# Optimization experiments

Hardware: AMD Instinct MI355X
Metric: run time of the kernel (lower is better)

The kernel has to match this reference:

```python
import jax, jax.numpy as jnp
import numpy as np

B, T, H = 1024, 1024, 64


def _lstm_cell(x, h, c, w_ih, w_hh, b_ih, b_hh):
    # gates: [B, 4H] in PyTorch order i, f, g, o
    g = x @ w_ih.T + h @ w_hh.T + b_ih + b_hh
    i, f, gg, o = jnp.split(g, 4, axis=-1)
    i = jax.nn.sigmoid(i)
    f = jax.nn.sigmoid(f)
    gg = jnp.tanh(gg)
    o = jax.nn.sigmoid(o)
    c_new = f * c + i * gg
    h_new = o * jnp.tanh(c_new)
    return h_new, c_new


def setup_inputs() -> dict:
    key = jax.random.key(0)
    ks = jax.random.split(key, 12)
    s = 1.0 / np.sqrt(H)  # torch default init scale
    r = lambda k, shape: jax.random.normal(k, shape, dtype=jnp.float32) * s
    return {
        "x": jax.random.normal(ks[0], (B, T), dtype=jnp.float32),
        "w_ih1": r(ks[1], (4 * H, 1)),
        "w_hh1": r(ks[2], (4 * H, H)),
        "b_ih1": r(ks[3], (4 * H,)),
        "b_hh1": r(ks[4], (4 * H,)),
        "w_ih2": r(ks[5], (4 * H, H)),
        "w_hh2": r(ks[6], (4 * H, H)),
        "b_ih2": r(ks[7], (4 * H,)),
        "b_hh2": r(ks[8], (4 * H,)),
        "w_lin": r(ks[9], (1, H)),
        "b_lin": r(ks[10], (1,)),
        "future_preds": 0,
    }


def reference(x, w_ih1, w_hh1, b_ih1, b_hh1, w_ih2, w_hh2, b_ih2, b_hh2,
              w_lin, b_lin, future_preds):
    bsz = x.shape[0]
    h1 = jnp.zeros((bsz, H), x.dtype)
    c1 = jnp.zeros((bsz, H), x.dtype)
    h2 = jnp.zeros((bsz, H), x.dtype)
    c2 = jnp.zeros((bsz, H), x.dtype)

    def step(carry, x_t):
        h1, c1, h2, c2 = carry
        h1, c1 = _lstm_cell(x_t, h1, c1, w_ih1, w_hh1, b_ih1, b_hh1)
        h2, c2 = _lstm_cell(h1, h2, c2, w_ih2, w_hh2, b_ih2, b_hh2)
        out = h2 @ w_lin.T + b_lin  # [B, 1]
        return (h1, c1, h2, c2), out

    xs = x.T[:, :, None]  # [T, B, 1]
    carry, outs = jax.lax.scan(step, (h1, c1, h2, c2), xs)
    outputs = outs[:, :, 0].T  # [B, T]

    if future_preds > 0:
        last = outs[-1]  # [B, 1]

        def fstep(carry, _):
            h1, c1, h2, c2, prev = carry
            h1, c1 = _lstm_cell(prev, h1, c1, w_ih1, w_hh1, b_ih1, b_hh1)
            h2, c2 = _lstm_cell(h1, h2, c2, w_ih2, w_hh2, b_ih2, b_hh2)
            out = h2 @ w_lin.T + b_lin
            return (h1, c1, h2, c2, out), out

        _, fouts = jax.lax.scan(fstep, (*carry, last), None, length=future_preds)
        outputs = jnp.concatenate([outputs, fouts[:, :, 0].T], axis=1)

    return outputs
```

## Files before the change

### kernel.cpp

```cpp
#include <hip/hip_runtime.h>
#include <hip/hip_bf16.h>


typedef _Float16 f16x8 __attribute__((ext_vector_type(8)));
typedef float    f32x4 __attribute__((ext_vector_type(4)));

namespace {
constexpr int Bb = 1024;
constexpr int Tt = 1024;
constexpr int NBat = 4;
constexpr int HSTR = 72;
constexpr int XSTR = 1025;
constexpr int SSTR = 20;

__device__ __forceinline__ float sigm(float x) {
    float e = __builtin_amdgcn_exp2f(-1.4426950408889634f * x);
    return __builtin_amdgcn_rcpf(1.0f + e);
}
__device__ __forceinline__ float tanh_f(float x) {
    float e = __builtin_amdgcn_exp2f(-2.8853900817779268f * x);
    return __builtin_amdgcn_rcpf(1.0f + e) * 2.0f - 1.0f;
}
__device__ __forceinline__ bool detect_f32(const void* w) {
    const unsigned short* p = (const unsigned short*)w;
    int sane = 0;
    for (int i = 0; i < 64; ++i) {
        int e = (p[2 * i] >> 7) & 0xFF;
        if (e >= 107 && e <= 129) ++sane;
    }
    return sane < 32;
}
__device__ __forceinline__ float ld(const void* p, int i, bool f32) {
    return f32 ? ((const float*)p)[i]
               : __bfloat162float(((const __hip_bfloat16*)p)[i]);
}
__device__ __forceinline__ void st(void* p, int i, float v, bool f32) {
    if (f32) ((float*)p)[i] = v;
    else     ((__hip_bfloat16*)p)[i] = __float2bfloat16(v);
}
}

__global__ __launch_bounds__(256, 1) void lstm2_kernel(
    const void* __restrict__ x,
    const void* __restrict__ w_ih1,
    const void* __restrict__ w_hh1,
    const void* __restrict__ b_ih1,
    const void* __restrict__ b_hh1,
    const void* __restrict__ w_ih2,
    const void* __restrict__ w_hh2,
    const void* __restrict__ b_ih2,
    const void* __restrict__ b_hh2,
    const void* __restrict__ w_lin,
    const void* __restrict__ b_lin,
    void* __restrict__ out)
{
    const int tid  = threadIdx.x;
    const int lane = tid & 63;
    const int w    = tid >> 6;
    const int m    = lane & 15;
    const int quad = lane >> 4;
    const int bb   = blockIdx.x * NBat;

    const bool f32 = detect_f32(w_hh1);

    __shared__ float                 xs[NBat * XSTR];
    __shared__ __align__(16) _Float16 h1buf[2][16 * HSTR];
    __shared__ __align__(16) _Float16 h2buf[2][16 * HSTR];
    __shared__ __align__(16) float    scr1[4][16 * SSTR];
    __shared__ __align__(16) float    scr2[4][16 * SSTR];
    __shared__ float                 headl[2][16];

    for (int i = tid; i < NBat * 1024; i += 256)
        xs[(i >> 10) * XSTR + (i & 1023)] = ld(x, (bb + (i >> 10)) * Tt + (i & 1023), f32);
    for (int i = tid; i < 16 * HSTR; i += 256) {
        h1buf[0][i] = (_Float16)0; h1buf[1][i] = (_Float16)0;
        h2buf[0][i] = (_Float16)0; h2buf[1][i] = (_Float16)0;
    }

    f16x8 wf1[4][2], wf2[4][2], wf3[4][2];
    if (f32) {
        const float* W1 = (const float*)w_hh1;
        const float* W2 = (const float*)w_ih2;
        const float* W3 = (const float*)w_hh2;
#pragma unroll
        for (int q = 0; q < 4; ++q) {
            const int row = 64 * q + 16 * w + m;
#pragma unroll
            for (int s = 0; s < 2; ++s) {
                const int base = row * 64 + 32 * s + quad * 8;
#pragma unroll
                for (int j = 0; j < 8; ++j) {
                    wf1[q][s][j] = (_Float16)W1[base + j];
                    wf2[q][s][j] = (_Float16)W2[base + j];
                    wf3[q][s][j] = (_Float16)W3[base + j];
                }
            }
        }
    } else {
        const __hip_bfloat16* W1 = (const __hip_bfloat16*)w_hh1;
        const __hip_bfloat16* W2 = (const __hip_bfloat16*)w_ih2;
        const __hip_bfloat16* W3 = (const __hip_bfloat16*)w_hh2;
#pragma unroll
        for (int q = 0; q < 4; ++q) {
            const int row = 64 * q + 16 * w + m;
#pragma unroll
            for (int s = 0; s < 2; ++s) {
                const int base = row * 64 + 32 * s + quad * 8;
#pragma unroll
                for (int j = 0; j < 8; ++j) {
                    wf1[q][s][j] = (_Float16)__bfloat162float(W1[base + j]);
                    wf2[q][s][j] = (_Float16)__bfloat162float(W2[base + j]);
                    wf3[q][s][j] = (_Float16)__bfloat162float(W3[base + j]);
                }
            }
        }
    }
    f32x4 b1v[4], b2v[4], wxv[4];
#pragma unroll
    for (int q = 0; q < 4; ++q)
#pragma unroll
        for (int r = 0; r < 4; ++r) {
            const int row = 64 * q + 16 * w + quad * 4 + r;
            b1v[q][r] = ld(b_ih1, row, f32) + ld(b_hh1, row, f32);
            b2v[q][r] = ld(b_ih2, row, f32) + ld(b_hh2, row, f32);
            wxv[q][r] = ld(w_ih1, row, f32);
        }
    const int cb = lane >> 4;
    const int uo = lane & 15;
    const float wl_u = ld(w_lin, 16 * w + uo, f32);
    const float blin = ld(b_lin, 0, f32);
    float c1 = 0.0f, c2 = 0.0f;
    __syncthreads();

    if (m < NBat) {
        const float x0 = xs[m * XSTR];
#pragma unroll
        for (int q = 0; q < 4; ++q) {
            f32x4 v;
#pragma unroll
            for (int r = 0; r < 4; ++r) v[r] = fmaf(x0, wxv[q][r], b1v[q][r]);
            *(f32x4*)&scr1[w][(q * 4 + m) * SSTR + quad * 4] = v;
        }
    }

    for (int t = 0; t < Tt; ++t) {
        const int cur = t & 1;
        {
            float gi = scr1[w][(0 * 4 + cb) * SSTR + uo];
            float gf = scr1[w][(1 * 4 + cb) * SSTR + uo];
            float gz = scr1[w][(2 * 4 + cb) * SSTR + uo];
            float go = scr1[w][(3 * 4 + cb) * SSTR + uo];
            float ig = sigm(gi), fg = sigm(gf), gg = tanh_f(gz), og = sigm(go);
            c1 = fmaf(fg, c1, ig * gg);
            h1buf[cur][cb * HSTR + 16 * w + uo] = (_Float16)(og * tanh_f(c1));
        }
        if (t > 0) {
            float gi = scr2[w][(0 * 4 + cb) * SSTR + uo];
            float gf = scr2[w][(1 * 4 + cb) * SSTR + uo];
            float gz = scr2[w][(2 * 4 + cb) * SSTR + uo];
            float go = scr2[w][(3 * 4 + cb) * SSTR + uo];
            float ig = sigm(gi), fg = sigm(gf), gg = tanh_f(gz), og = sigm(go);
            c2 = fmaf(fg, c2, ig * gg);
            float h = og * tanh_f(c2);
            h2buf[cur][cb * HSTR + 16 * w + uo] = (_Float16)h;
            float p = h * wl_u;
            p += __shfl_xor(p, 1); p += __shfl_xor(p, 2);
            p += __shfl_xor(p, 4); p += __shfl_xor(p, 8);
            if (uo == 0) headl[cur][w * 4 + cb] = p;
        }
        __syncthreads();

        if (t > 0 && tid < NBat) {
            float s = blin;
#pragma unroll
            for (int k = 0; k < 4; ++k) s += headl[cur][k * 4 + tid];
            st(out, (bb + tid) * Tt + (t - 1), s, f32);
        }
        const f16x8 bh1a = *(const f16x8*)(h1buf[cur] + m * HSTR + quad * 8);
        const f16x8 bh1b = *(const f16x8*)(h1buf[cur] + m * HSTR + 32 + quad * 8);
        const f16x8 bh2a = *(const f16x8*)(h2buf[cur] + m * HSTR + quad * 8);
        const f16x8 bh2b = *(const f16x8*)(h2buf[cur] + m * HSTR + 32 + quad * 8);
        const float xtn  = xs[(m & (NBat - 1)) * XSTR + ((t + 1 < Tt) ? t + 1 : t)];
#pragma unroll
        for (int q = 0; q < 4; ++q) {
            f32x4 a2 = __builtin_amdgcn_mfma_f32_16x16x32_f16(wf2[q][0], bh1a, b2v[q], 0, 0, 0);
            a2 = __builtin_amdgcn_mfma_f32_16x16x32_f16(wf2[q][1], bh1b, a2, 0, 0, 0);
            a2 = __builtin_amdgcn_mfma_f32_16x16x32_f16(wf3[q][0], bh2a, a2, 0, 0, 0);
            a2 = __builtin_amdgcn_mfma_f32_16x16x32_f16(wf3[q][1], bh2b, a2, 0, 0, 0);
            f32x4 a1;
#pragma unroll
            for (int r = 0; r < 4; ++r) a1[r] = fmaf(xtn, wxv[q][r], b1v[q][r]);
            a1 = __builtin_amdgcn_mfma_f32_16x16x32_f16(wf1[q][0], bh1a, a1, 0, 0, 0);
            a1 = __builtin_amdgcn_mfma_f32_16x16x32_f16(wf1[q][1], bh1b, a1, 0, 0, 0);
            if (m < NBat) {
                *(f32x4*)&scr2[w][(q * 4 + m) * SSTR + quad * 4] = a2;
                *(f32x4*)&scr1[w][(q * 4 + m) * SSTR + quad * 4] = a1;
            }
        }
    }

    {
        float gi = scr2[w][(0 * 4 + cb) * SSTR + uo];
        float gf = scr2[w][(1 * 4 + cb) * SSTR + uo];
        float gz = scr2[w][(2 * 4 + cb) * SSTR + uo];
        float go = scr2[w][(3 * 4 + cb) * SSTR + uo];
        float ig = sigm(gi), fg = sigm(gf), gg = tanh_f(gz), og = sigm(go);
        c2 = fmaf(fg, c2, ig * gg);
        float h = og * tanh_f(c2);
        float p = h * wl_u;
        p += __shfl_xor(p, 1); p += __shfl_xor(p, 2);
        p += __shfl_xor(p, 4); p += __shfl_xor(p, 8);
        if (uo == 0) headl[0][w * 4 + cb] = p;
    }
    __syncthreads();
    if (tid < NBat) {
        float s = blin;
#pragma unroll
        for (int k = 0; k < 4; ++k) s += headl[0][k * 4 + tid];
        st(out, (bb + tid) * Tt + (Tt - 1), s, f32);
    }
}

extern "C" void kernel_launch(void* const* d_in, const int* in_sizes, int n_in,
                              void* d_out, int out_size, void* d_ws, size_t ws_size,
                              hipStream_t stream)
{
    (void)in_sizes; (void)n_in; (void)out_size; (void)d_ws; (void)ws_size;
    lstm2_kernel<<<dim3(Bb / NBat), dim3(256), 0, stream>>>(
        d_in[0], d_in[1], d_in[2], d_in[3], d_in[4], d_in[5],
        d_in[6], d_in[7], d_in[8], d_in[9], d_in[10], d_out);
}
```

Baseline: 892.2 us.

## Transpose gate scratch layout for vector reads and split MFMA chains

Stores the per-step gate pre-activations in a transposed shared-memory layout so each lane reads its four gates (i,f,g,o) with one 128-bit load instead of four scalar loads. The layer-2 MFMA accumulation is split into two independent chains that are summed at the end, which shortens the serial dependency on the critical recurrent path. The head output store is moved after the MFMAs so it overlaps with matrix work. The transposed stores now pack values across q, which adds register shuffling and four vector stores per lane in place of the previous ones.

After: 1.089 ms. +22.0%, slower.

```diff
diff --git a/kernel.cpp b/kernel.cpp
--- a/kernel.cpp
+++ b/kernel.cpp
@@ -11,7 +11,6 @@
 constexpr int NBat = 4;
 constexpr int HSTR = 72;
 constexpr int XSTR = 1025;
-constexpr int SSTR = 20;
 
 __device__ __forceinline__ float sigm(float x) {
     float e = __builtin_amdgcn_exp2f(-1.4426950408889634f * x);
@@ -63,12 +62,12 @@
 
     const bool f32 = detect_f32(w_hh1);
 
-    __shared__ float                 xs[NBat * XSTR];
+    __shared__ float                  xs[NBat * XSTR];
     __shared__ __align__(16) _Float16 h1buf[2][16 * HSTR];
     __shared__ __align__(16) _Float16 h2buf[2][16 * HSTR];
-    __shared__ __align__(16) float    scr1[4][16 * SSTR];
-    __shared__ __align__(16) float    scr2[4][16 * SSTR];
-    __shared__ float                 headl[2][16];
+    __shared__ __align__(16) float    scrT1[4][NBat * 16 * 4];
+    __shared__ __align__(16) float    scrT2[4][NBat * 16 * 4];
+    __shared__ float                  headl[2][16];
 
     for (int i = tid; i < NBat * 1024; i += 256)
         xs[(i >> 10) * XSTR + (i & 1023)] = ld(x, (bb + (i >> 10)) * Tt + (i & 1023), f32);
@@ -127,6 +126,7 @@
         }
     const int cb = lane >> 4;
     const int uo = lane & 15;
+    const int cidx = (cb * 16 + uo) * 4;
     const float wl_u = ld(w_lin, 16 * w + uo, f32);
     const float blin = ld(b_lin, 0, f32);
     float c1 = 0.0f, c2 = 0.0f;
@@ -135,31 +135,27 @@
     if (m < NBat) {
         const float x0 = xs[m * XSTR];
 #pragma unroll
-        for (int q = 0; q < 4; ++q) {
+        for (int r = 0; r < 4; ++r) {
             f32x4 v;
 #pragma unroll
-            for (int r = 0; r < 4; ++r) v[r] = fmaf(x0, wxv[q][r], b1v[q][r]);
-            *(f32x4*)&scr1[w][(q * 4 + m) * SSTR + quad * 4] = v;
+            for (int q = 0; q < 4; ++q) v[q] = fmaf(x0, wxv[q][r], b1v[q][r]);
+            *(f32x4*)&scrT1[w][(m * 16 + quad * 4 + r) * 4] = v;
         }
     }
 
     for (int t = 0; t < Tt; ++t) {
         const int cur = t & 1;
         {
-            float gi = scr1[w][(0 * 4 + cb) * SSTR + uo];
-            float gf = scr1[w][(1 * 4 + cb) * SSTR + uo];
-            float gz = scr1[w][(2 * 4 + cb) * SSTR + uo];
-            float go = scr1[w][(3 * 4 + cb) * SSTR + uo];
-            float ig = sigm(gi), fg = sigm(gf), gg = tanh_f(gz), og = sigm(go);
+            const f32x4 g = *(const f32x4*)&scrT1[w][cidx];
+            float ig = sigm(g[0]), fg = sigm(g[1]);
+            float gg = tanh_f(g[2]), og = sigm(g[3]);
             c1 = fmaf(fg, c1, ig * gg);
             h1buf[cur][cb * HSTR + 16 * w + uo] = (_Float16)(og * tanh_f(c1));
         }
         if (t > 0) {
-            float gi = scr2[w][(0 * 4 + cb) * SSTR + uo];
-            float gf = scr2[w][(1 * 4 + cb) * SSTR + uo];
-            float gz = scr2[w][(2 * 4 + cb) * SSTR + uo];
-            float go = scr2[w][(3 * 4 + cb) * SSTR + uo];
-            float ig = sigm(gi), fg = sigm(gf), gg = tanh_f(gz), og = sigm(go);
+            const f32x4 g = *(const f32x4*)&scrT2[w][cidx];
+            float ig = sigm(g[0]), fg = sigm(g[1]);
+            float gg = tanh_f(g[2]), og = sigm(g[3]);
             c2 = fmaf(fg, c2, ig * gg);
             float h = og * tanh_f(c2);
             h2buf[cur][cb * HSTR + 16 * w + uo] = (_Float16)h;
@@ -170,41 +166,45 @@
         }
         __syncthreads();
 
-        if (t > 0 && tid < NBat) {
-            float s = blin;
-#pragma unroll
-            for (int k = 0; k < 4; ++k) s += headl[cur][k * 4 + tid];
-            st(out, (bb + tid) * Tt + (t - 1), s, f32);
-        }
         const f16x8 bh1a = *(const f16x8*)(h1buf[cur] + m * HSTR + quad * 8);
         const f16x8 bh1b = *(const f16x8*)(h1buf[cur] + m * HSTR + 32 + quad * 8);
         const f16x8 bh2a = *(const f16x8*)(h2buf[cur] + m * HSTR + quad * 8);
         const f16x8 bh2b = *(const f16x8*)(h2buf[cur] + m * HSTR + 32 + quad * 8);
         const float xtn  = xs[(m & (NBat - 1)) * XSTR + ((t + 1 < Tt) ? t + 1 : t)];
+        f32x4 a1[4], a2[4];
 #pragma unroll
         for (int q = 0; q < 4; ++q) {
-            f32x4 a2 = __builtin_amdgcn_mfma_f32_16x16x32_f16(wf2[q][0], bh1a, b2v[q], 0, 0, 0);
-            a2 = __builtin_amdgcn_mfma_f32_16x16x32_f16(wf2[q][1], bh1b, a2, 0, 0, 0);
-            a2 = __builtin_amdgcn_mfma_f32_16x16x32_f16(wf3[q][0], bh2a, a2, 0, 0, 0);
-            a2 = __builtin_amdgcn_mfma_f32_16x16x32_f16(wf3[q][1], bh2b, a2, 0, 0, 0);
-            f32x4 a1;
-#pragma unroll
-            for (int r = 0; r < 4; ++r) a1[r] = fmaf(xtn, wxv[q][r], b1v[q][r]);
-            a1 = __builtin_amdgcn_mfma_f32_16x16x32_f16(wf1[q][0], bh1a, a1, 0, 0, 0);
-            a1 = __builtin_amdgcn_mfma_f32_16x16x32_f16(wf1[q][1], bh1b, a1, 0, 0, 0);
-            if (m < NBat) {
-                *(f32x4*)&scr2[w][(q * 4 + m) * SSTR + quad * 4] = a2;
-                *(f32x4*)&scr1[w][(q * 4 + m) * SSTR + quad * 4] = a1;
+            f32x4 p2 = __builtin_amdgcn_mfma_f32_16x16x32_f16(wf2[q][0], bh1a, b2v[q], 0, 0, 0);
+            p2 = __builtin_amdgcn_mfma_f32_16x16x32_f16(wf2[q][1], bh1b, p2, 0, 0, 0);
+            f32x4 p3 = __builtin_amdgcn_mfma_f32_16x16x32_f16(wf3[q][0], bh2a, f32x4{0,0,0,0}, 0, 0, 0);
+            p3 = __builtin_amdgcn_mfma_f32_16x16x32_f16(wf3[q][1], bh2b, p3, 0, 0, 0);
+            f32x4 i1;
+#pragma unroll
+            for (int r = 0; r < 4; ++r) i1[r] = fmaf(xtn, wxv[q][r], b1v[q][r]);
+            i1 = __builtin_amdgcn_mfma_f32_16x16x32_f16(wf1[q][0], bh1a, i1, 0, 0, 0);
+            a1[q] = __builtin_amdgcn_mfma_f32_16x16x32_f16(wf1[q][1], bh1b, i1, 0, 0, 0);
+            a2[q] = p2 + p3;
+        }
+        if (t > 0 && tid < NBat) {
+            float s = blin;
+#pragma unroll
+            for (int k = 0; k < 4; ++k) s += headl[cur][k * 4 + tid];
+            st(out, (bb + tid) * Tt + (t - 1), s, f32);
+        }
+        if (m < NBat) {
+#pragma unroll
+            for (int r = 0; r < 4; ++r) {
+                const int idx = (m * 16 + quad * 4 + r) * 4;
+                *(f32x4*)&scrT2[w][idx] = f32x4{a2[0][r], a2[1][r], a2[2][r], a2[3][r]};
+                *(f32x4*)&scrT1[w][idx] = f32x4{a1[0][r], a1[1][r], a1[2][r], a1[3][r]};
             }
         }
     }
 
     {
-        float gi = scr2[w][(0 * 4 + cb) * SSTR + uo];
-        float gf = scr2[w][(1 * 4 + cb) * SSTR + uo];
-        float gz = scr2[w][(2 * 4 + cb) * SSTR + uo];
-        float go = scr2[w][(3 * 4 + cb) * SSTR + uo];
-        float ig = sigm(gi), fg = sigm(gf), gg = tanh_f(gz), og = sigm(go);
+        const f32x4 g = *(const f32x4*)&scrT2[w][cidx];
+        float ig = sigm(g[0]), fg = sigm(g[1]);
+        float gg = tanh_f(g[2]), og = sigm(g[3]);
         c2 = fmaf(fg, c2, ig * gg);
         float h = og * tanh_f(c2);
         float p = h * wl_u;
```
